# Performance work log

Hardware: AMD Instinct MI355X
Metric: run time of the kernel (lower is better)

Reference implementation:

```python
import jax, jax.numpy as jnp
import numpy as np

B, C, T = 8, 256, 2048
DS = 4
SC = C // DS          # tsa_scale = 64
DEPTH = 256           # temporal_depth (band width)
BN_EPS = 1e-5


def _conv_bn_relu(x, W, b, g, beta, mu, var):
    # 1x1 conv on [B, C, T, 1] layout == channel matmul, then eval-mode BN, then ReLU
    y = jnp.einsum('bctz,oc->botz', x, W) + b[None, :, None, None]
    inv = g / jnp.sqrt(var + BN_EPS)
    y = (y - mu[None, :, None, None]) * inv[None, :, None, None] + beta[None, :, None, None]
    return jax.nn.relu(y)


def setup_inputs() -> dict:
    key = jax.random.key(0)
    ks = jax.random.split(key, 20)
    inp = {"x": jax.random.normal(ks[0], (B, C, T, 1), jnp.float32)}
    for name, oc, base in (("k", SC, 1), ("q", SC, 7), ("v", C, 13)):
        inp[name + "W"] = jax.random.normal(ks[base], (oc, C), jnp.float32) * 0.05
        inp[name + "b"] = jax.random.normal(ks[base + 1], (oc,), jnp.float32) * 0.05
        inp[name + "g"] = 1.0 + 0.05 * jax.random.normal(ks[base + 2], (oc,), jnp.float32)
        inp[name + "beta"] = jax.random.normal(ks[base + 3], (oc,), jnp.float32) * 0.05
        inp[name + "mu"] = jax.random.normal(ks[base + 4], (oc,), jnp.float32) * 0.05
        inp[name + "var"] = 1.0 + 0.1 * jax.random.uniform(ks[base + 5], (oc,), jnp.float32)
    return inp


def reference(x, kW, kb, kg, kbeta, kmu, kvar,
              qW, qb, qg, qbeta, qmu, qvar,
              vW, vb, vg, vbeta, vmu, vvar):
    key = _conv_bn_relu(x, kW, kb, kg, kbeta, kmu, kvar)[..., 0]                      # [B, SC, T]
    query = _conv_bn_relu(x, qW, qb, qg, qbeta, qmu, qvar)[..., 0].transpose(0, 2, 1)  # [B, T, SC]
    value = _conv_bn_relu(x, vW, vb, vg, vbeta, vmu, vvar)[..., 0].transpose(0, 2, 1)  # [B, T, C]

    i = jnp.arange(T)
    # tril(diag=0) * triu(diag=-(DEPTH-1)): causal band of width DEPTH
    mask = ((i[:, None] >= i[None, :]) & (i[:, None] - i[None, :] <= DEPTH - 1)).astype(x.dtype)

    s = jnp.einsum('btd,bds->bts', query, key) * mask / np.float32(np.sqrt(SC))
    s = jnp.exp(s - jnp.max(s, axis=2, keepdims=True)) * mask
    # NOTE: original torch code does `torch.sum(...)[0]`, indexing batch 0 of the
    # sum tensor ([T,1]) and broadcasting it across the batch. Replicated faithfully.
    s = s / (jnp.sum(s, axis=2, keepdims=True)[0] + 1e-30)

    tsa_out = jnp.einsum('bts,bsc->btc', s, value)                                     # [B, T, C]
    return x + tsa_out.transpose(0, 2, 1)[..., None]                                   # res_skip
```

## Files before the change

kernel.cpp:

```cpp
#include <hip/hip_runtime.h>

#define TDIM 2048

typedef __bf16 bf16_t;
typedef bf16_t bf16x8 __attribute__((ext_vector_type(8)));
typedef float f32x4 __attribute__((ext_vector_type(4)));
typedef unsigned short us8 __attribute__((ext_vector_type(8)));

__device__ __forceinline__ unsigned short f2bf(float x) {
  unsigned u = __builtin_bit_cast(unsigned, x);
  u += 0x7fffu + ((u >> 16) & 1u);
  return (unsigned short)(u >> 16);
}

__device__ __forceinline__ void gl_lds16(const unsigned short* g, unsigned short* l) {
  __builtin_amdgcn_global_load_lds(
      (const __attribute__((address_space(1))) unsigned int*)g,
      (__attribute__((address_space(3))) unsigned int*)l, 16, 0, 0);
}

__global__ __launch_bounds__(256) void k_prepw(
    const float* __restrict__ kW, const float* __restrict__ kb,
    const float* __restrict__ kg, const float* __restrict__ kbe,
    const float* __restrict__ kmu, const float* __restrict__ kva,
    const float* __restrict__ qW, const float* __restrict__ qb,
    const float* __restrict__ qg, const float* __restrict__ qbe,
    const float* __restrict__ qmu, const float* __restrict__ qva,
    const float* __restrict__ vW, const float* __restrict__ vb,
    const float* __restrict__ vg, const float* __restrict__ vbe,
    const float* __restrict__ vmu, const float* __restrict__ vva,
    unsigned short* __restrict__ effWf,
    float* __restrict__ effb)
{
  const int idx = blockIdx.x;
  const int tid = threadIdx.x;
  const int gid = idx >> 2, cc = idx & 3;
  unsigned short* dst = effWf + (size_t)idx * 8192;
#pragma unroll
  for (int pass = 0; pass < 4; ++pass) {
    int f = pass * 256 + tid;
    int ocblk = f >> 7, cblk = (f >> 4) & 7, m = f & 15;
    int G = gid * 128 + ocblk * 16 + m;
    const float* Wp = (G < 64) ? (kW + G * 256)
                     : (G < 128) ? (qW + (G - 64) * 256)
                                 : (vW + (G - 128) * 256);
    float gg = (G < 64) ? kg[G]  : (G < 128) ? qg[G - 64]  : vg[G - 128];
    float vr = (G < 64) ? kva[G] : (G < 128) ? qva[G - 64] : vva[G - 128];
    float inv = gg * rsqrtf(vr + 1e-5f);
    int c = cc * 64 + cblk * 8;
    float4 a = *(const float4*)(Wp + c);
    float4 bq = *(const float4*)(Wp + c + 4);
    ushort4 lo, hi;
    lo.x = f2bf(a.x * inv);  lo.y = f2bf(a.y * inv);
    lo.z = f2bf(a.z * inv);  lo.w = f2bf(a.w * inv);
    hi.x = f2bf(bq.x * inv); hi.y = f2bf(bq.y * inv);
    hi.z = f2bf(bq.z * inv); hi.w = f2bf(bq.w * inv);
    *(ushort4*)(dst + f * 8) = lo;
    *(ushort4*)(dst + f * 8 + 4) = hi;
  }
  if (idx == 0) {
    for (int G = tid; G < 384; G += 256) {
      float gg = (G < 64) ? kg[G]  : (G < 128) ? qg[G - 64]  : vg[G - 128];
      float vr = (G < 64) ? kva[G] : (G < 128) ? qva[G - 64] : vva[G - 128];
      float bb = (G < 64) ? kb[G]  : (G < 128) ? qb[G - 64]  : vb[G - 128];
      float mm = (G < 64) ? kmu[G] : (G < 128) ? qmu[G - 64] : vmu[G - 128];
      float be = (G < 64) ? kbe[G] : (G < 128) ? qbe[G - 64] : vbe[G - 128];
      float inv = gg * rsqrtf(vr + 1e-5f);
      effb[G] = (bb - mm) * inv + be;
    }
  }
}

__global__ __launch_bounds__(256, 3) void k_qkv(
    const unsigned short* __restrict__ effWf,
    const float* __restrict__ effb,
    const float* __restrict__ x,
    unsigned short* __restrict__ vv,
    unsigned short* __restrict__ kTs,
    unsigned short* __restrict__ qTs)
{
  const int tb = blockIdx.x, gid = blockIdx.y, b = blockIdx.z;
  const int tid = threadIdx.x;
  const int lane = tid & 63, wv = tid >> 6;
  const int m = lane & 15, quad = lane >> 4;
  const int t0 = tb * 64;

  __shared__ unsigned short Wb[2][8192];
  __shared__ unsigned short Xs[4608];
  __shared__ float effbs[128];

  if (tid < 128) effbs[tid] = effb[gid * 128 + tid];

  const unsigned short* wbase = effWf + (size_t)gid * 32768;
  const float* xb = x + (size_t)b * 256 * TDIM + t0 + lane;

  float xr[16];

  auto stageW = [&](int cc, int bufi) {
    const unsigned short* ws = wbase + cc * 8192;
#pragma unroll
    for (int i = 0; i < 4; ++i) {
      int ii = wv * 4 + i;
      gl_lds16(ws + (ii * 64 + lane) * 8, &Wb[bufi][ii * 512]);
    }
  };
  auto loadX = [&](int cc) {
#pragma unroll
    for (int p = 0; p < 4; ++p)
#pragma unroll
      for (int j = 0; j < 4; ++j) {
        int c = cc * 64 + p * 16 + wv * 4 + j;
        xr[p * 4 + j] = xb[(size_t)c * TDIM];
      }
  };

  const f32x4 fz = {0.f, 0.f, 0.f, 0.f};
  f32x4 acc[2][4];
#pragma unroll
  for (int i = 0; i < 2; ++i)
#pragma unroll
    for (int j = 0; j < 4; ++j) acc[i][j] = fz;

  stageW(0, 0);
  loadX(0);
  for (int cc = 0; cc < 4; ++cc) {
    __syncthreads();
#pragma unroll
    for (int p = 0; p < 4; ++p) {
      int cb4 = p * 16 + wv * 4;
      int swz = (((cb4 >> 3) ^ (lane >> 3)) << 3) | (cb4 & 7);
      ushort4 s4;
      s4.x = f2bf(xr[p * 4 + 0]); s4.y = f2bf(xr[p * 4 + 1]);
      s4.z = f2bf(xr[p * 4 + 2]); s4.w = f2bf(xr[p * 4 + 3]);
      *(ushort4*)&Xs[lane * 72 + swz] = s4;
    }
    if (cc < 3) { stageW(cc + 1, (cc + 1) & 1); loadX(cc + 1); }
    __syncthreads();
    const unsigned short* Wc = Wb[cc & 1];
#pragma unroll
    for (int kk = 0; kk < 2; ++kk) {
      int cb = kk * 4 + quad;
      bf16x8 af[2], bfv[4];
#pragma unroll
      for (int mt = 0; mt < 2; ++mt)
        af[mt] = *(const bf16x8*)&Wc[(((wv * 2 + mt) * 8 + cb) * 16 + m) * 8];
#pragma unroll
      for (int nt = 0; nt < 4; ++nt) {
        int t = nt * 16 + m;
        bfv[nt] = *(const bf16x8*)&Xs[t * 72 + ((cb ^ (t >> 3)) << 3)];
      }
#pragma unroll
      for (int mt = 0; mt < 2; ++mt)
#pragma unroll
        for (int nt = 0; nt < 4; ++nt)
          acc[mt][nt] = __builtin_amdgcn_mfma_f32_16x16x32_bf16(af[mt], bfv[nt], acc[mt][nt], 0, 0, 0);
    }
  }

  if (gid == 0) {
#pragma unroll
    for (int mt = 0; mt < 2; ++mt)
#pragma unroll
      for (int nt = 0; nt < 4; ++nt) {
        int ocl = wv * 32 + mt * 16 + quad * 4;
        int t = t0 + nt * 16 + m;
        ushort4 s4;
        s4.x = f2bf(fmaxf(acc[mt][nt][0] + effbs[ocl + 0], 0.f));
        s4.y = f2bf(fmaxf(acc[mt][nt][1] + effbs[ocl + 1], 0.f));
        s4.z = f2bf(fmaxf(acc[mt][nt][2] + effbs[ocl + 2], 0.f));
        s4.w = f2bf(fmaxf(acc[mt][nt][3] + effbs[ocl + 3], 0.f));
        if (ocl < 64) {
          int col = (((ocl >> 3) ^ (t & 7)) << 3) | (ocl & 7);
          *(ushort4*)(kTs + ((size_t)(b * TDIM + t)) * 64 + col) = s4;
        } else {
          int oq = ocl - 64;
          int col = (((oq >> 3) ^ (t & 7)) << 3) | (oq & 7);
          *(ushort4*)(qTs + ((size_t)(b * TDIM + t)) * 64 + col) = s4;
        }
      }
  } else {
#pragma unroll
    for (int mt = 0; mt < 2; ++mt)
#pragma unroll
      for (int nt = 0; nt < 4; ++nt)
#pragma unroll
        for (int r = 0; r < 4; ++r) {
          int ocl = wv * 32 + mt * 16 + quad * 4 + r;
          float y = fmaxf(acc[mt][nt][r] + effbs[ocl], 0.f);
          int c = (gid - 1) * 128 + ocl;
          int t = t0 + nt * 16 + m;
          vv[(size_t)(b * 256 + c) * TDIM + t] = f2bf(y);
        }
  }
}

__global__ __launch_bounds__(512, 1) void k_denom(
    const unsigned short* __restrict__ kTs,
    const unsigned short* __restrict__ qTs,
    float* __restrict__ denom0)
{
  const int t0d = blockIdx.x * 16;
  const int tid = threadIdx.x;
  const int lane = tid & 63, w = tid >> 6;
  const int m = lane & 15, quad = lane >> 4;

  __shared__ unsigned short S[18432];
  unsigned short* Qs = S;
  unsigned short* Ks = S + 1024;
  __shared__ float pmaxs[8][16];
  __shared__ float psums[8][16];

  {
    const unsigned short* qg = qTs + (size_t)t0d * 64;
    const unsigned short* kg = kTs + ((long)t0d - 256) * 64;
#pragma unroll
    for (int it = 0; it < 5; ++it) {
      int j = it * 512 + tid;
      if (j < 2304) {
        const unsigned short* g = (j < 128) ? (qg + j * 8) : (kg + (size_t)(j - 128) * 8);
        gl_lds16(g, &S[(it * 512 + w * 64) * 8]);
      }
    }
  }
  __syncthreads();

  const int jn = (w == 0) ? 3 : 2;
  f32x4 sc[3];
  {
    int t = m;
    bf16x8 qf0 = *(const bf16x8*)&Qs[t * 64 + ((quad ^ (t & 7)) << 3)];
    bf16x8 qf1 = *(const bf16x8*)&Qs[t * 64 + (((4 + quad) ^ (t & 7)) << 3)];
    const f32x4 fz = {0.f, 0.f, 0.f, 0.f};
#pragma unroll
    for (int jj = 0; jj < 3; ++jj) {
      if (jj < jn) {
        int j = w + jj * 8;
        int sr = 16 * j + m;
        f32x4 a = fz;
        bf16x8 kf0 = *(const bf16x8*)&Ks[sr * 64 + ((quad ^ (sr & 7)) << 3)];
        a = __builtin_amdgcn_mfma_f32_16x16x32_bf16(qf0, kf0, a, 0, 0, 0);
        bf16x8 kf1 = *(const bf16x8*)&Ks[sr * 64 + (((4 + quad) ^ (sr & 7)) << 3)];
        a = __builtin_amdgcn_mfma_f32_16x16x32_bf16(qf1, kf1, a, 0, 0, 0);
        sc[jj] = a;
      }
    }
  }

  float mx[4] = {0.f, 0.f, 0.f, 0.f};
#pragma unroll
  for (int jj = 0; jj < 3; ++jj)
    if (jj < jn) {
      int j = w + jj * 8;
#pragma unroll
      for (int r = 0; r < 4; ++r) {
        float v = sc[jj][r] * 0.125f;
        sc[jj][r] = v;
        int tg = t0d + quad * 4 + r;
        int sg = t0d - 256 + 16 * j + m;
        if (sg >= 0 && sg <= tg && tg - sg < 256) mx[r] = fmaxf(mx[r], v);
      }
    }
#pragma unroll
  for (int d = 1; d < 16; d <<= 1)
#pragma unroll
    for (int r = 0; r < 4; ++r) mx[r] = fmaxf(mx[r], __shfl_xor(mx[r], d, 64));
  if (m == 0)
#pragma unroll
    for (int r = 0; r < 4; ++r) pmaxs[w][quad * 4 + r] = mx[r];
  __syncthreads();

  float mxf[4];
#pragma unroll
  for (int r = 0; r < 4; ++r) {
    float v = pmaxs[0][quad * 4 + r];
#pragma unroll
    for (int ww = 1; ww < 8; ++ww) v = fmaxf(v, pmaxs[ww][quad * 4 + r]);
    mxf[r] = v;
  }
  float sm[4] = {0.f, 0.f, 0.f, 0.f};
#pragma unroll
  for (int jj = 0; jj < 3; ++jj)
    if (jj < jn) {
      int j = w + jj * 8;
#pragma unroll
      for (int r = 0; r < 4; ++r) {
        int tg = t0d + quad * 4 + r;
        int sg = t0d - 256 + 16 * j + m;
        if (sg >= 0 && sg <= tg && tg - sg < 256) sm[r] += __expf(sc[jj][r] - mxf[r]);
      }
    }
#pragma unroll
  for (int d = 1; d < 16; d <<= 1)
#pragma unroll
    for (int r = 0; r < 4; ++r) sm[r] += __shfl_xor(sm[r], d, 64);
  if (m == 0)
#pragma unroll
    for (int r = 0; r < 4; ++r) psums[w][quad * 4 + r] = sm[r];
  __syncthreads();

  if (tid < 16) {
    float s = 0.f;
#pragma unroll
    for (int ww = 0; ww < 8; ++ww) s += psums[ww][tid];
    denom0[t0d + tid] = s;
  }
}

__global__ __launch_bounds__(512, 2) void k_attn(
    const float* __restrict__ x,
    const unsigned short* __restrict__ vv,
    const unsigned short* __restrict__ kTs,
    const unsigned short* __restrict__ qTs,
    const float* __restrict__ denom0,
    float* __restrict__ out)
{
  const int bx = blockIdx.x, b = blockIdx.y;
  const int tb = (bx >> 3) + 4 * (bx & 7);
  const int tid = threadIdx.x;
  const int lane = tid & 63, w = tid >> 6;
  const int m = lane & 15, quad = lane >> 4;
  const int t0 = tb * 64;

  __shared__ unsigned short SM[24576];
  __shared__ float pmaxs[128];
  unsigned short* Qs = SM;
  unsigned short* Ks = SM + 4096;
  unsigned short* Ps = SM;

  {
    const unsigned short* qg = qTs + ((size_t)(b * TDIM + t0)) * 64;
    const unsigned short* kg = kTs + ((long)(b * TDIM + t0) - 256) * 64;
#pragma unroll
    for (int it = 0; it < 6; ++it) {
      int j = it * 512 + tid;
      const unsigned short* g = (j < 512) ? (qg + (size_t)j * 8)
                                          : (kg + (size_t)(j - 512) * 8);
      gl_lds16(g, &SM[(it * 512 + w * 64) * 8]);
    }
  }
  const int rt = w & 3, half = w >> 2;
  const int tw = t0 + rt * 16;
  float dval[4];
#pragma unroll
  for (int r = 0; r < 4; ++r) dval[r] = denom0[tw + quad * 4 + r];
  __syncthreads();

  const int j0 = half ? 9 : 0;
  const int jn = half ? 8 : 9;
  f32x4 sc[9];
  {
    int t = rt * 16 + m;
    bf16x8 qf0 = *(const bf16x8*)&Qs[t * 64 + ((quad ^ (t & 7)) << 3)];
    bf16x8 qf1 = *(const bf16x8*)&Qs[t * 64 + (((4 + quad) ^ (t & 7)) << 3)];
    const f32x4 fz = {0.f, 0.f, 0.f, 0.f};
#pragma unroll
    for (int jj = 0; jj < 9; ++jj) {
      if (jj < jn) {
        int sr = 16 * (rt + j0 + jj) + m;
        f32x4 a = fz;
        bf16x8 kf0 = *(const bf16x8*)&Ks[sr * 64 + ((quad ^ (sr & 7)) << 3)];
        a = __builtin_amdgcn_mfma_f32_16x16x32_bf16(qf0, kf0, a, 0, 0, 0);
        bf16x8 kf1 = *(const bf16x8*)&Ks[sr * 64 + (((4 + quad) ^ (sr & 7)) << 3)];
        a = __builtin_amdgcn_mfma_f32_16x16x32_bf16(qf1, kf1, a, 0, 0, 0);
        sc[jj] = a;
      }
    }
  }

  float mx[4] = {0.f, 0.f, 0.f, 0.f};
#pragma unroll
  for (int jj = 0; jj < 9; ++jj)
    if (jj < jn) {
#pragma unroll
      for (int r = 0; r < 4; ++r) {
        float v = sc[jj][r] * 0.125f;
        sc[jj][r] = v;
        int tg = tw + quad * 4 + r;
        int sg = t0 - 256 + 16 * (rt + j0 + jj) + m;
        if (sg >= 0 && sg <= tg && tg - sg < 256) mx[r] = fmaxf(mx[r], v);
      }
    }
#pragma unroll
  for (int d = 1; d < 16; d <<= 1)
#pragma unroll
    for (int r = 0; r < 4; ++r) mx[r] = fmaxf(mx[r], __shfl_xor(mx[r], d, 64));
  if (m == 0)
#pragma unroll
    for (int r = 0; r < 4; ++r) pmaxs[half * 64 + rt * 16 + quad * 4 + r] = mx[r];

  __syncthreads();

  float mxf[4], rden[4];
#pragma unroll
  for (int r = 0; r < 4; ++r) {
    int row = rt * 16 + quad * 4 + r;
    mxf[r] = fmaxf(pmaxs[row], pmaxs[64 + row]);
    rden[r] = 1.f / (dval[r] + 1e-30f);
  }
#pragma unroll
  for (int jj = 0; jj < 9; ++jj)
    if (jj < jn) {
#pragma unroll
      for (int r = 0; r < 4; ++r) {
        int tg = tw + quad * 4 + r;
        int sg = t0 - 256 + 16 * (rt + j0 + jj) + m;
        bool ib = (sg >= 0 && sg <= tg && tg - sg < 256);
        sc[jj][r] = ib ? __expf(sc[jj][r] - mxf[r]) * rden[r] : 0.f;
      }
    }

  if (half == 0) {
    if (rt > 0) {
      int row = rt * 16 + (lane >> 2), col = 16 * rt - 16 + (lane & 3) * 4;
      ushort4 z; z.x = 0; z.y = 0; z.z = 0; z.w = 0;
      *(ushort4*)&Ps[row * 344 + col] = z;
    }
  } else {
    if (rt < 3) {
      int row = rt * 16 + (lane >> 2), col = 16 * rt + 272 + (lane & 3) * 4;
      ushort4 z; z.x = 0; z.y = 0; z.z = 0; z.w = 0;
      *(ushort4*)&Ps[row * 344 + col] = z;
    }
  }
#pragma unroll
  for (int jj = 0; jj < 9; ++jj)
    if (jj < jn) {
      int col = 16 * (rt + j0 + jj) + m;
#pragma unroll
      for (int r = 0; r < 4; ++r)
        Ps[(rt * 16 + quad * 4 + r) * 344 + col] = f2bf(sc[jj][r]);
    }

  const int cbase = w * 32;
  const unsigned short* vrow0 = vv + (size_t)(b * 256 + cbase + m) * TDIM;
  const unsigned short* vrow1 = vrow0 + (size_t)16 * TDIM;
  us8 vreg0 = {0, 0, 0, 0, 0, 0, 0, 0}, vreg1 = {0, 0, 0, 0, 0, 0, 0, 0};
  if (t0 >= 256) {
    vreg0 = *(const us8*)(vrow0 + t0 - 256 + quad * 8);
    vreg1 = *(const us8*)(vrow1 + t0 - 256 + quad * 8);
  }

  __syncthreads();

  float4 xv[4][2];
#pragma unroll
  for (int mt = 0; mt < 4; ++mt)
#pragma unroll
    for (int ct = 0; ct < 2; ++ct) {
      int c = cbase + ct * 16 + m;
      int t = t0 + mt * 16 + quad * 4;
      xv[mt][ct] = *(const float4*)(x + (size_t)(b * 256 + c) * TDIM + t);
    }

  const f32x4 fz = {0.f, 0.f, 0.f, 0.f};
  f32x4 acc[4][2];
#pragma unroll
  for (int i = 0; i < 4; ++i) { acc[i][0] = fz; acc[i][1] = fz; }
#pragma unroll
  for (int chunk = 0; chunk < 10; ++chunk) {
    us8 vn0 = {0, 0, 0, 0, 0, 0, 0, 0}, vn1 = {0, 0, 0, 0, 0, 0, 0, 0};
    if (chunk < 9) {
      int sbase = t0 - 256 + (chunk + 1) * 32;
      if (sbase >= 0) {
        vn0 = *(const us8*)(vrow0 + sbase + quad * 8);
        vn1 = *(const us8*)(vrow1 + sbase + quad * 8);
      }
    }
    bf16x8 bfr0 = __builtin_bit_cast(bf16x8, vreg0);
    bf16x8 bfr1 = __builtin_bit_cast(bf16x8, vreg1);
#pragma unroll
    for (int mt = 0; mt < 4; ++mt) {
      const int cs = mt >> 1;
      if (chunk >= cs && chunk <= cs + 8) {
        bf16x8 af = *(const bf16x8*)&Ps[(mt * 16 + m) * 344 + chunk * 32 + quad * 8];
        acc[mt][0] = __builtin_amdgcn_mfma_f32_16x16x32_bf16(af, bfr0, acc[mt][0], 0, 0, 0);
        acc[mt][1] = __builtin_amdgcn_mfma_f32_16x16x32_bf16(af, bfr1, acc[mt][1], 0, 0, 0);
      }
    }
    vreg0 = vn0; vreg1 = vn1;
  }

#pragma unroll
  for (int mt = 0; mt < 4; ++mt)
#pragma unroll
    for (int ct = 0; ct < 2; ++ct) {
      int c = cbase + ct * 16 + m;
      int t = t0 + mt * 16 + quad * 4;
      size_t off = (size_t)(b * 256 + c) * TDIM + t;
      float4 o;
      o.x = xv[mt][ct].x + acc[mt][ct][0];
      o.y = xv[mt][ct].y + acc[mt][ct][1];
      o.z = xv[mt][ct].z + acc[mt][ct][2];
      o.w = xv[mt][ct].w + acc[mt][ct][3];
      *(float4*)(out + off) = o;
    }
}

extern "C" void kernel_launch(void* const* d_in, const int* in_sizes, int n_in,
                              void* d_out, int out_size, void* d_ws, size_t ws_size,
                              hipStream_t stream) {
  const float* x   = (const float*)d_in[0];
  const float* kW  = (const float*)d_in[1];
  const float* kb  = (const float*)d_in[2];
  const float* kg  = (const float*)d_in[3];
  const float* kbe = (const float*)d_in[4];
  const float* kmu = (const float*)d_in[5];
  const float* kva = (const float*)d_in[6];
  const float* qW  = (const float*)d_in[7];
  const float* qb  = (const float*)d_in[8];
  const float* qg  = (const float*)d_in[9];
  const float* qbe = (const float*)d_in[10];
  const float* qmu = (const float*)d_in[11];
  const float* qva = (const float*)d_in[12];
  const float* vW  = (const float*)d_in[13];
  const float* vb  = (const float*)d_in[14];
  const float* vg  = (const float*)d_in[15];
  const float* vbe = (const float*)d_in[16];
  const float* vmu = (const float*)d_in[17];
  const float* vva = (const float*)d_in[18];

  unsigned short* vv  = (unsigned short*)d_ws;
  unsigned short* kTs = vv + (size_t)8 * 256 * TDIM;
  unsigned short* qTs = kTs + (size_t)8 * TDIM * 64;
  float* denom0 = (float*)(qTs + (size_t)8 * TDIM * 64);
  unsigned short* effWf = (unsigned short*)(denom0 + 2048);
  float* effb = (float*)(effWf + 12 * 8192);
  float* outp = (float*)d_out;

  k_prepw<<<dim3(12), 256, 0, stream>>>(
      kW, kb, kg, kbe, kmu, kva,
      qW, qb, qg, qbe, qmu, qva,
      vW, vb, vg, vbe, vmu, vva, effWf, effb);
  k_qkv<<<dim3(32, 3, 8), 256, 0, stream>>>(effWf, effb, x, vv, kTs, qTs);
  k_denom<<<dim3(128), 512, 0, stream>>>(kTs, qTs, denom0);
  k_attn<<<dim3(32, 8), 512, 0, stream>>>(x, vv, kTs, qTs, denom0, outp);
}
```

Measured before the change: 132.3 us.

## Halve attention query tile to 32 rows and double grid for occupancy

```diff
diff --git a/kernel.cpp b/kernel.cpp
--- a/kernel.cpp
+++ b/kernel.cpp
@@ -306,7 +306,7 @@
   }
 }
 
-__global__ __launch_bounds__(512, 2) void k_attn(
+__global__ __launch_bounds__(512, 4) void k_attn(
     const float* __restrict__ x,
     const unsigned short* __restrict__ vv,
     const unsigned short* __restrict__ kTs,
@@ -314,47 +314,46 @@
     const float* __restrict__ denom0,
     float* __restrict__ out)
 {
-  const int bx = blockIdx.x, b = blockIdx.y;
-  const int tb = (bx >> 3) + 4 * (bx & 7);
+  const int tb = blockIdx.x, b = blockIdx.y;
   const int tid = threadIdx.x;
   const int lane = tid & 63, w = tid >> 6;
   const int m = lane & 15, quad = lane >> 4;
-  const int t0 = tb * 64;
-
-  __shared__ unsigned short SM[24576];
-  __shared__ float pmaxs[128];
+  const int t0 = tb * 32;
+
+  __shared__ unsigned short SM[20480];
+  __shared__ float pmaxs[4][32];
   unsigned short* Qs = SM;
-  unsigned short* Ks = SM + 4096;
+  unsigned short* Ks = SM + 2048;
   unsigned short* Ps = SM;
 
   {
-    const unsigned short* qg = qTs + ((size_t)(b * TDIM + t0)) * 64;
+    const unsigned short* qg = qTs + (size_t)(b * TDIM + t0) * 64;
     const unsigned short* kg = kTs + ((long)(b * TDIM + t0) - 256) * 64;
 #pragma unroll
-    for (int it = 0; it < 6; ++it) {
+    for (int it = 0; it < 5; ++it) {
       int j = it * 512 + tid;
-      const unsigned short* g = (j < 512) ? (qg + (size_t)j * 8)
-                                          : (kg + (size_t)(j - 512) * 8);
+      const unsigned short* g = (j < 256) ? qg + (size_t)j * 8
+                                          : kg + (size_t)(j - 256) * 8;
       gl_lds16(g, &SM[(it * 512 + w * 64) * 8]);
     }
   }
-  const int rt = w & 3, half = w >> 2;
+  const int rt = w & 1, part = w >> 1;
   const int tw = t0 + rt * 16;
   float dval[4];
 #pragma unroll
   for (int r = 0; r < 4; ++r) dval[r] = denom0[tw + quad * 4 + r];
   __syncthreads();
 
-  const int j0 = half ? 9 : 0;
-  const int jn = half ? 8 : 9;
-  f32x4 sc[9];
+  const int j0 = (part == 0) ? 0 : (part == 1) ? 5 : (part == 2) ? 9 : 13;
+  const int jn = (part == 0) ? 5 : 4;
+  f32x4 sc[5];
   {
     int t = rt * 16 + m;
     bf16x8 qf0 = *(const bf16x8*)&Qs[t * 64 + ((quad ^ (t & 7)) << 3)];
     bf16x8 qf1 = *(const bf16x8*)&Qs[t * 64 + (((4 + quad) ^ (t & 7)) << 3)];
     const f32x4 fz = {0.f, 0.f, 0.f, 0.f};
 #pragma unroll
-    for (int jj = 0; jj < 9; ++jj) {
+    for (int jj = 0; jj < 5; ++jj)
       if (jj < jn) {
         int sr = 16 * (rt + j0 + jj) + m;
         f32x4 a = fz;
@@ -364,12 +363,11 @@
         a = __builtin_amdgcn_mfma_f32_16x16x32_bf16(qf1, kf1, a, 0, 0, 0);
         sc[jj] = a;
       }
-    }
   }
 
   float mx[4] = {0.f, 0.f, 0.f, 0.f};
 #pragma unroll
-  for (int jj = 0; jj < 9; ++jj)
+  for (int jj = 0; jj < 5; ++jj)
     if (jj < jn) {
 #pragma unroll
       for (int r = 0; r < 4; ++r) {
@@ -386,7 +384,7 @@
     for (int r = 0; r < 4; ++r) mx[r] = fmaxf(mx[r], __shfl_xor(mx[r], d, 64));
   if (m == 0)
 #pragma unroll
-    for (int r = 0; r < 4; ++r) pmaxs[half * 64 + rt * 16 + quad * 4 + r] = mx[r];
+    for (int r = 0; r < 4; ++r) pmaxs[part][rt * 16 + quad * 4 + r] = mx[r];
 
   __syncthreads();
 
@@ -394,11 +392,12 @@
 #pragma unroll
   for (int r = 0; r < 4; ++r) {
     int row = rt * 16 + quad * 4 + r;
-    mxf[r] = fmaxf(pmaxs[row], pmaxs[64 + row]);
+    mxf[r] = fmaxf(fmaxf(pmaxs[0][row], pmaxs[1][row]),
+                   fmaxf(pmaxs[2][row], pmaxs[3][row]));
     rden[r] = 1.f / (dval[r] + 1e-30f);
   }
 #pragma unroll
-  for (int jj = 0; jj < 9; ++jj)
+  for (int jj = 0; jj < 5; ++jj)
     if (jj < jn) {
 #pragma unroll
       for (int r = 0; r < 4; ++r) {
@@ -409,26 +408,19 @@
       }
     }
 
-  if (half == 0) {
-    if (rt > 0) {
-      int row = rt * 16 + (lane >> 2), col = 16 * rt - 16 + (lane & 3) * 4;
-      ushort4 z; z.x = 0; z.y = 0; z.z = 0; z.w = 0;
-      *(ushort4*)&Ps[row * 344 + col] = z;
-    }
-  } else {
-    if (rt < 3) {
-      int row = rt * 16 + (lane >> 2), col = 16 * rt + 272 + (lane & 3) * 4;
-      ushort4 z; z.x = 0; z.y = 0; z.z = 0; z.w = 0;
-      *(ushort4*)&Ps[row * 344 + col] = z;
-    }
-  }
-#pragma unroll
-  for (int jj = 0; jj < 9; ++jj)
+  if (part == 1) {
+    int row = rt * 16 + (lane >> 2);
+    int col = (rt == 0) ? (272 + (lane & 3) * 4) : ((lane & 3) * 4);
+    ushort4 z; z.x = 0; z.y = 0; z.z = 0; z.w = 0;
+    *(ushort4*)&Ps[row * 296 + col] = z;
+  }
+#pragma unroll
+  for (int jj = 0; jj < 5; ++jj)
     if (jj < jn) {
       int col = 16 * (rt + j0 + jj) + m;
 #pragma unroll
       for (int r = 0; r < 4; ++r)
-        Ps[(rt * 16 + quad * 4 + r) * 344 + col] = f2bf(sc[jj][r]);
+        Ps[(rt * 16 + quad * 4 + r) * 296 + col] = f2bf(sc[jj][r]);
     }
 
   const int cbase = w * 32;
@@ -442,9 +434,9 @@
 
   __syncthreads();
 
-  float4 xv[4][2];
-#pragma unroll
-  for (int mt = 0; mt < 4; ++mt)
+  float4 xv[2][2];
+#pragma unroll
+  for (int mt = 0; mt < 2; ++mt)
 #pragma unroll
     for (int ct = 0; ct < 2; ++ct) {
       int c = cbase + ct * 16 + m;
@@ -453,13 +445,12 @@
     }
 
   const f32x4 fz = {0.f, 0.f, 0.f, 0.f};
-  f32x4 acc[4][2];
-#pragma unroll
-  for (int i = 0; i < 4; ++i) { acc[i][0] = fz; acc[i][1] = fz; }
-#pragma unroll
-  for (int chunk = 0; chunk < 10; ++chunk) {
+  f32x4 acc[2][2];
+  acc[0][0] = fz; acc[0][1] = fz; acc[1][0] = fz; acc[1][1] = fz;
+#pragma unroll
+  for (int chunk = 0; chunk < 9; ++chunk) {
     us8 vn0 = {0, 0, 0, 0, 0, 0, 0, 0}, vn1 = {0, 0, 0, 0, 0, 0, 0, 0};
-    if (chunk < 9) {
+    if (chunk < 8) {
       int sbase = t0 - 256 + (chunk + 1) * 32;
       if (sbase >= 0) {
         vn0 = *(const us8*)(vrow0 + sbase + quad * 8);
@@ -469,19 +460,16 @@
     bf16x8 bfr0 = __builtin_bit_cast(bf16x8, vreg0);
     bf16x8 bfr1 = __builtin_bit_cast(bf16x8, vreg1);
 #pragma unroll
-    for (int mt = 0; mt < 4; ++mt) {
-      const int cs = mt >> 1;
-      if (chunk >= cs && chunk <= cs + 8) {
-        bf16x8 af = *(const bf16x8*)&Ps[(mt * 16 + m) * 344 + chunk * 32 + quad * 8];
-        acc[mt][0] = __builtin_amdgcn_mfma_f32_16x16x32_bf16(af, bfr0, acc[mt][0], 0, 0, 0);
-        acc[mt][1] = __builtin_amdgcn_mfma_f32_16x16x32_bf16(af, bfr1, acc[mt][1], 0, 0, 0);
-      }
+    for (int mt = 0; mt < 2; ++mt) {
+      bf16x8 af = *(const bf16x8*)&Ps[(mt * 16 + m) * 296 + chunk * 32 + quad * 8];
+      acc[mt][0] = __builtin_amdgcn_mfma_f32_16x16x32_bf16(af, bfr0, acc[mt][0], 0, 0, 0);
+      acc[mt][1] = __builtin_amdgcn_mfma_f32_16x16x32_bf16(af, bfr1, acc[mt][1], 0, 0, 0);
     }
     vreg0 = vn0; vreg1 = vn1;
   }
 
 #pragma unroll
-  for (int mt = 0; mt < 4; ++mt)
+  for (int mt = 0; mt < 2; ++mt)
 #pragma unroll
     for (int ct = 0; ct < 2; ++ct) {
       int c = cbase + ct * 16 + m;
@@ -533,5 +521,5 @@
       vW, vb, vg, vbe, vmu, vva, effWf, effb);
   k_qkv<<<dim3(32, 3, 8), 256, 0, stream>>>(effWf, effb, x, vv, kTs, qTs);
   k_denom<<<dim3(128), 512, 0, stream>>>(kTs, qTs, denom0);
-  k_attn<<<dim3(32, 8), 512, 0, stream>>>(x, vv, kTs, qTs, denom0, outp);
-}
+  k_attn<<<dim3(64, 8), 512, 0, stream>>>(x, vv, kTs, qTs, denom0, outp);
+}
```

After: 136.4 us. 1.03x slower.
